# Kernel optimization log

Measured on AMD Instinct MI355X. Metric: run time of the kernel, lower is better.

The kernel has to match this reference:

```python
import jax, jax.numpy as jnp
import numpy as np

B, A, D, H = 16384, 16, 512, 512


def setup_inputs() -> dict:
    key = jax.random.key(0)
    ks = jax.random.split(key, 8)
    s = 1.0 / np.sqrt(D)
    sh = 1.0 / np.sqrt(H)
    return {
        "state": jax.random.normal(ks[0], (B, D), jnp.float32),
        "W1": jax.random.normal(ks[1], (A, D, H), jnp.float32) * s,
        "b1": jax.random.normal(ks[2], (A, H), jnp.float32) * s,
        "W2": jax.random.normal(ks[3], (A, H, H), jnp.float32) * sh,
        "b2": jax.random.normal(ks[4], (A, H), jnp.float32) * sh,
        "W3": jax.random.normal(ks[5], (A, H, 1), jnp.float32) * sh,
        "b3": jax.random.normal(ks[6], (A, 1), jnp.float32) * sh,
        "actions": jax.random.randint(ks[7], (B,), 0, A, jnp.int64),
    }


def reference(state, W1, b1, W2, b2, W3, b3, actions):
    # All per-action MLPs applied to every state as grouped/batched GEMMs.
    # h1, h2: [B, A, H]; out: [B, A, n_out]
    h1 = jax.nn.relu(jnp.einsum("bd,adh->bah", state, W1) + b1)
    h2 = jax.nn.relu(jnp.einsum("bah,ahk->bak", h1, W2) + b2)
    out = jnp.einsum("bah,ahk->bak", h2, W3) + b3  # [B, A, 1]
    # Gather the selected action's output per batch element -> [B, n_out]
    return jnp.take_along_axis(out, actions[:, None, None], axis=1)[:, 0, :]
```

## Files before the change

### kernel.cpp

```cpp
#include <hip/hip_runtime.h>
#include <hip/hip_bf16.h>
#include <stdint.h>

typedef __hip_bfloat16 bf16;
typedef float f32x4 __attribute__((ext_vector_type(4)));
typedef short bf16x8 __attribute__((ext_vector_type(8)));

#define NB 16384
#define NA 16
#define ND 512
#define NH 512
#define TR 80

#define W1S_OFF 0u
#define W2S_OFF 8388608u
#define PERM_OFF 16777216u
#define META_OFF 16842752u

__device__ __forceinline__ unsigned short f2b(float x) {
  unsigned int b = __float_as_uint(x);
  return (unsigned short)((b + 0x7FFFu + ((b >> 16) & 1u)) >> 16);
}

__global__ __launch_bounds__(256) void k_prep(const float* __restrict__ W1,
                                              const float* __restrict__ W2,
                                              bf16* __restrict__ W1s,
                                              bf16* __restrict__ W2s,
                                              const int* __restrict__ act,
                                              int* __restrict__ meta,
                                              int* __restrict__ perm) {
  __shared__ union {
    float tile[64][65];
    struct { int hist[16][256]; int off16[16]; } m;
  } lds;
  if (blockIdx.x == 2048) {
    int t = threadIdx.x;
    int lane = t & 63, wv = t >> 6;
#pragma unroll
    for (int i = 0; i < 16; ++i) lds.m.hist[i][t] = 0;
    __syncthreads();
    for (int j = 0; j < 64; ++j) {
      int a = act[t + (j << 8)] & 15;
      lds.m.hist[a][t]++;
    }
    __syncthreads();
    for (int q = 0; q < 4; ++q) {
      int a = (wv << 2) + q;
      int base = lane << 2;
      int v0 = lds.m.hist[a][base + 0];
      int v1 = lds.m.hist[a][base + 1];
      int v2 = lds.m.hist[a][base + 2];
      int v3 = lds.m.hist[a][base + 3];
      int s = v0 + v1 + v2 + v3;
      int incl = s;
#pragma unroll
      for (int d = 1; d < 64; d <<= 1) {
        int y = __shfl_up(incl, d);
        if (lane >= d) incl += y;
      }
      int excl = incl - s;
      lds.m.hist[a][base + 0] = excl;
      lds.m.hist[a][base + 1] = excl + v0;
      lds.m.hist[a][base + 2] = excl + v0 + v1;
      lds.m.hist[a][base + 3] = excl + v0 + v1 + v2;
      if (lane == 63) lds.m.off16[a] = incl;
    }
    __syncthreads();
    if (t == 0) {
      int o = 0;
      for (int aa = 0; aa < 16; ++aa) {
        int c = lds.m.off16[aa];
        meta[aa] = c;
        meta[16 + aa] = o;
        lds.m.off16[aa] = o;
        o += c;
      }
    }
    __syncthreads();
    for (int j = 0; j < 64; ++j) {
      int idx = t + (j << 8);
      int a = act[idx] & 15;
      int pos = lds.m.off16[a] + lds.m.hist[a][t]++;
      perm[pos] = idx;
    }
    return;
  }
  int j = blockIdx.x;
  int xcd = j & 7;
  int job = j >> 3;
  int mi = job >> 6;
  int m = (mi < 2) ? ((xcd << 1) + mi) : (NA + (xcd << 1) + (mi - 2));
  int tl = job & 63;
  int td = tl >> 3, th = tl & 7;
  const float* src = (m < NA) ? (W1 + (size_t)m * (ND * NH)) : (W2 + (size_t)(m - NA) * (ND * NH));
  char* dstb = (m < NA) ? ((char*)W1s + ((size_t)m << 19)) : ((char*)W2s + ((size_t)(m - NA) << 19));
  int t = threadIdx.x;
  int r = t >> 2, c0 = (t & 3) << 4;
  const float* sp = src + (size_t)(td * 64 + r) * NH + th * 64 + c0;
  float4 v0 = ((const float4*)sp)[0];
  float4 v1 = ((const float4*)sp)[1];
  float4 v2 = ((const float4*)sp)[2];
  float4 v3 = ((const float4*)sp)[3];
  float* tr = &lds.tile[r][c0];
  tr[0] = v0.x; tr[1] = v0.y; tr[2] = v0.z; tr[3] = v0.w;
  tr[4] = v1.x; tr[5] = v1.y; tr[6] = v1.z; tr[7] = v1.w;
  tr[8] = v2.x; tr[9] = v2.y; tr[10] = v2.z; tr[11] = v2.w;
  tr[12] = v3.x; tr[13] = v3.y; tr[14] = v3.z; tr[15] = v3.w;
  __syncthreads();
  int wv = t >> 6, l = t & 63;
  int l15b = l & 15, l4b = l >> 4;
#pragma unroll
  for (int kc = 0; kc < 2; ++kc) {
    union { unsigned short us[8]; uint4 q; } u;
#pragma unroll
    for (int i = 0; i < 8; ++i)
      u.us[i] = f2b(lds.tile[kc * 32 + l4b * 8 + i][wv * 16 + l15b]);
    int hb = th * 4 + wv;
    int kb = td * 2 + kc;
    *(uint4*)(dstb + ((size_t)(hb * 16 + kb) << 10) + (l << 4)) = u.q;
  }
}

__global__ __launch_bounds__(1024, 4) void k_main(
    const float* __restrict__ state, const float* __restrict__ b1,
    const float* __restrict__ b2, const float* __restrict__ W3,
    const float* __restrict__ b3, const bf16* __restrict__ W1s,
    const bf16* __restrict__ W2s, const int* __restrict__ perm,
    const int* __restrict__ meta, float* __restrict__ out) {
  extern __shared__ char smem[];
  char* Xs = smem;
  float* outbuf = (float*)(smem + 81920);

  int bid = blockIdx.x;
  int xcd = bid & 7, slot = bid >> 3;
  int a0 = xcd << 1;
  int n0 = meta[a0], n1 = meta[a0 + 1];
  int nt0 = (n0 + TR - 1) / TR, nt1 = (n1 + TR - 1) / TR;
  int a, t;
  if (slot < nt0) {
    a = a0; t = slot;
  } else if (slot < nt0 + nt1) {
    a = a0 + 1; t = slot - nt0;
  } else {
    return;
  }
  int rowbase = meta[16 + a] + t * TR;
  int nrows = meta[a] - t * TR;
  nrows = nrows > TR ? TR : nrows;

  int tid = threadIdx.x;
  int lane = tid & 63;
  int w = tid >> 6;
  int hw = w & 7;
  int ch = w >> 3;
  int bf0 = ch ? 3 : 0;
  int bfn = ch ? 2 : 3;
  int l15 = lane & 15, l4 = lane >> 4;

  const char* Wl = (const char*)W1s + ((size_t)a << 19) + (hw << 16) + (lane << 4);
  const char* Wl2 = (const char*)W2s + ((size_t)a << 19) + (hw << 16) + (lane << 4);

  bf16x8 A[2][4];
  bf16x8 Bc[3];
#pragma unroll
  for (int s = 0; s < 2; ++s)
#pragma unroll
    for (int hf = 0; hf < 4; ++hf)
      A[s][hf] = *(const bf16x8*)(Wl + (hf << 14) + (s << 10));

  {
#pragma unroll
    for (int it = 0; it < 10; ++it) {
      int c = tid + (it << 10);
      int row = c >> 7, chunk = c & 127;
      int gr = (row < nrows) ? perm[rowbase + row] : -1;
      float4 v = make_float4(0.f, 0.f, 0.f, 0.f);
      if (gr >= 0) v = *(const float4*)(state + (size_t)gr * ND + (chunk << 2));
      uint2 pk;
      pk.x = (unsigned)f2b(v.x) | ((unsigned)f2b(v.y) << 16);
      pk.y = (unsigned)f2b(v.z) | ((unsigned)f2b(v.w) << 16);
      *(uint2*)(Xs + row * 1024 + ((chunk << 3) ^ ((row & 7) << 4))) = pk;
    }
  }
  __syncthreads();

  uint2 h1p[12];

  {
    f32x4 acc[4][3] = {};
#pragma unroll
    for (int ks = 0; ks < 16; ++ks) {
#pragma unroll
      for (int bf = 0; bf < 3; ++bf) {
        if (bf < bfn) {
          int b = ((bf0 + bf) << 4) + l15;
          Bc[bf] = *(const bf16x8*)(Xs + b * 1024 + (((ks << 6) + (l4 << 4)) ^ ((b & 7) << 4)));
        }
      }
      __builtin_amdgcn_s_setprio(1);
#pragma unroll
      for (int hf = 0; hf < 4; ++hf)
#pragma unroll
        for (int bf = 0; bf < 3; ++bf)
          if (bf < bfn)
            acc[hf][bf] = __builtin_amdgcn_mfma_f32_16x16x32_bf16(A[ks & 1][hf], Bc[bf], acc[hf][bf], 0, 0, 0);
      __builtin_amdgcn_s_setprio(0);
      if (ks < 14) {
#pragma unroll
        for (int hf = 0; hf < 4; ++hf)
          A[ks & 1][hf] = *(const bf16x8*)(Wl + (hf << 14) + ((ks + 2) << 10));
      }
    }
#pragma unroll
    for (int s = 0; s < 2; ++s)
#pragma unroll
      for (int hf = 0; hf < 4; ++hf)
        A[s][hf] = *(const bf16x8*)(Wl2 + (hf << 14) + (s << 10));
#pragma unroll
    for (int hf = 0; hf < 4; ++hf) {
      int hb = (hw << 6) + (hf << 4) + (l4 << 2);
      float4 bias = *(const float4*)(b1 + (a << 9) + hb);
#pragma unroll
      for (int bf = 0; bf < 3; ++bf) {
        if (bf < bfn) {
          float x0 = fmaxf(acc[hf][bf][0] + bias.x, 0.f);
          float x1 = fmaxf(acc[hf][bf][1] + bias.y, 0.f);
          float x2 = fmaxf(acc[hf][bf][2] + bias.z, 0.f);
          float x3 = fmaxf(acc[hf][bf][3] + bias.w, 0.f);
          h1p[hf * 3 + bf].x = (unsigned)f2b(x0) | ((unsigned)f2b(x1) << 16);
          h1p[hf * 3 + bf].y = (unsigned)f2b(x2) | ((unsigned)f2b(x3) << 16);
        }
      }
    }
  }
  __syncthreads();
#pragma unroll
  for (int hf = 0; hf < 4; ++hf) {
    int hb2 = ((hw << 6) + (hf << 4) + (l4 << 2)) << 1;
#pragma unroll
    for (int bf = 0; bf < 3; ++bf) {
      if (bf < bfn) {
        int b = ((bf0 + bf) << 4) + l15;
        *(uint2*)(Xs + b * 1024 + (hb2 ^ ((b & 7) << 4))) = h1p[hf * 3 + bf];
      }
    }
  }
  __syncthreads();

  {
    f32x4 acc[4][3] = {};
#pragma unroll
    for (int ks = 0; ks < 16; ++ks) {
#pragma unroll
      for (int bf = 0; bf < 3; ++bf) {
        if (bf < bfn) {
          int b = ((bf0 + bf) << 4) + l15;
          Bc[bf] = *(const bf16x8*)(Xs + b * 1024 + (((ks << 6) + (l4 << 4)) ^ ((b & 7) << 4)));
        }
      }
      __builtin_amdgcn_s_setprio(1);
#pragma unroll
      for (int hf = 0; hf < 4; ++hf)
#pragma unroll
        for (int bf = 0; bf < 3; ++bf)
          if (bf < bfn)
            acc[hf][bf] = __builtin_amdgcn_mfma_f32_16x16x32_bf16(A[ks & 1][hf], Bc[bf], acc[hf][bf], 0, 0, 0);
      __builtin_amdgcn_s_setprio(0);
      if (ks < 14) {
#pragma unroll
        for (int hf = 0; hf < 4; ++hf)
          A[ks & 1][hf] = *(const bf16x8*)(Wl2 + (hf << 14) + ((ks + 2) << 10));
      }
    }
    float part[3] = {0.f, 0.f, 0.f};
#pragma unroll
    for (int hf = 0; hf < 4; ++hf) {
      int hb = (hw << 6) + (hf << 4) + (l4 << 2);
      float4 bias = *(const float4*)(b2 + (a << 9) + hb);
      float4 w3v = *(const float4*)(W3 + (a << 9) + hb);
#pragma unroll
      for (int bf = 0; bf < 3; ++bf) {
        if (bf < bfn) {
          part[bf] += fmaxf(acc[hf][bf][0] + bias.x, 0.f) * w3v.x +
                      fmaxf(acc[hf][bf][1] + bias.y, 0.f) * w3v.y +
                      fmaxf(acc[hf][bf][2] + bias.z, 0.f) * w3v.z +
                      fmaxf(acc[hf][bf][3] + bias.w, 0.f) * w3v.w;
        }
      }
    }
#pragma unroll
    for (int bf = 0; bf < 3; ++bf) {
      if (bf < bfn) {
        float p = part[bf];
        p += __shfl_xor(p, 16);
        p += __shfl_xor(p, 32);
        if (l4 == 0) outbuf[w * TR + ((bf0 + bf) << 4) + l15] = p;
      }
    }
  }
  __syncthreads();
  if (tid < nrows) {
    float s = b3[a];
    int wb = (tid < 48) ? 0 : 8;
#pragma unroll
    for (int ww = 0; ww < 8; ++ww) s += outbuf[(wb + ww) * TR + tid];
    out[perm[rowbase + tid]] = s;
  }
}

extern "C" void kernel_launch(void* const* d_in, const int* in_sizes, int n_in,
                              void* d_out, int out_size, void* d_ws, size_t ws_size,
                              hipStream_t stream) {
  const float* state = (const float*)d_in[0];
  const float* W1 = (const float*)d_in[1];
  const float* b1 = (const float*)d_in[2];
  const float* W2 = (const float*)d_in[3];
  const float* b2 = (const float*)d_in[4];
  const float* W3 = (const float*)d_in[5];
  const float* b3 = (const float*)d_in[6];
  const int* actions = (const int*)d_in[7];
  float* out = (float*)d_out;
  char* ws = (char*)d_ws;
  bf16* W1s = (bf16*)(ws + W1S_OFF);
  bf16* W2s = (bf16*)(ws + W2S_OFF);
  int* perm = (int*)(ws + PERM_OFF);
  int* meta = (int*)(ws + META_OFF);

  k_prep<<<2049, 256, 0, stream>>>(W1, W2, W1s, W2s, actions, meta, perm);
  hipFuncSetAttribute((const void*)k_main, hipFuncAttributeMaxDynamicSharedMemorySize, 87040);
  k_main<<<256, 1024, 87040, stream>>>(state, b1, b2, W3, b3, W1s, W2s, perm, meta, out);
}
```

Baseline: 59.57 us.

## Shrink row tile to 48 with 512-thread blocks and double grid

Reduces the per-block row tile from 80 to 48 rows and the block size from 1024 to 512 threads, so each of 8 waves owns a 64-column H slice and processes all three 16-row B fragments uniformly. The grid doubles to 512 blocks and LDS per block shrinks. The aim is to remove the uneven split across wave halves and get more blocks resident per CU. In exchange, each weight tile is reused across fewer rows, so weight traffic per row goes up. The grid of 512 blocks must cover ceil(n/48) tiles per action pair on each XCD slot.

```diff
diff --git a/kernel.cpp b/kernel.cpp
--- a/kernel.cpp
+++ b/kernel.cpp
@@ -10,7 +10,7 @@
 #define NA 16
 #define ND 512
 #define NH 512
-#define TR 80
+#define TR 48
 
 #define W1S_OFF 0u
 #define W2S_OFF 8388608u
@@ -121,7 +121,7 @@
   }
 }
 
-__global__ __launch_bounds__(1024, 4) void k_main(
+__global__ __launch_bounds__(512, 2) void k_main(
     const float* __restrict__ state, const float* __restrict__ b1,
     const float* __restrict__ b2, const float* __restrict__ W3,
     const float* __restrict__ b3, const bf16* __restrict__ W1s,
@@ -129,7 +129,7 @@
     const int* __restrict__ meta, float* __restrict__ out) {
   extern __shared__ char smem[];
   char* Xs = smem;
-  float* outbuf = (float*)(smem + 81920);
+  float* outbuf = (float*)(smem + 49152);
 
   int bid = blockIdx.x;
   int xcd = bid & 7, slot = bid >> 3;
@@ -151,14 +151,10 @@
   int tid = threadIdx.x;
   int lane = tid & 63;
   int w = tid >> 6;
-  int hw = w & 7;
-  int ch = w >> 3;
-  int bf0 = ch ? 3 : 0;
-  int bfn = ch ? 2 : 3;
   int l15 = lane & 15, l4 = lane >> 4;
 
-  const char* Wl = (const char*)W1s + ((size_t)a << 19) + (hw << 16) + (lane << 4);
-  const char* Wl2 = (const char*)W2s + ((size_t)a << 19) + (hw << 16) + (lane << 4);
+  const char* Wl = (const char*)W1s + ((size_t)a << 19) + (w << 16) + (lane << 4);
+  const char* Wl2 = (const char*)W2s + ((size_t)a << 19) + (w << 16) + (lane << 4);
 
   bf16x8 A[2][4];
   bf16x8 Bc[3];
@@ -170,8 +166,8 @@
 
   {
 #pragma unroll
-    for (int it = 0; it < 10; ++it) {
-      int c = tid + (it << 10);
+    for (int it = 0; it < 12; ++it) {
+      int c = tid + (it << 9);
       int row = c >> 7, chunk = c & 127;
       int gr = (row < nrows) ? perm[rowbase + row] : -1;
       float4 v = make_float4(0.f, 0.f, 0.f, 0.f);
@@ -192,18 +188,15 @@
     for (int ks = 0; ks < 16; ++ks) {
 #pragma unroll
       for (int bf = 0; bf < 3; ++bf) {
-        if (bf < bfn) {
-          int b = ((bf0 + bf) << 4) + l15;
-          Bc[bf] = *(const bf16x8*)(Xs + b * 1024 + (((ks << 6) + (l4 << 4)) ^ ((b & 7) << 4)));
-        }
+        int b = (bf << 4) + l15;
+        Bc[bf] = *(const bf16x8*)(Xs + b * 1024 + (((ks << 6) + (l4 << 4)) ^ ((b & 7) << 4)));
       }
       __builtin_amdgcn_s_setprio(1);
 #pragma unroll
       for (int hf = 0; hf < 4; ++hf)
 #pragma unroll
         for (int bf = 0; bf < 3; ++bf)
-          if (bf < bfn)
-            acc[hf][bf] = __builtin_amdgcn_mfma_f32_16x16x32_bf16(A[ks & 1][hf], Bc[bf], acc[hf][bf], 0, 0, 0);
+          acc[hf][bf] = __builtin_amdgcn_mfma_f32_16x16x32_bf16(A[ks & 1][hf], Bc[bf], acc[hf][bf], 0, 0, 0);
       __builtin_amdgcn_s_setprio(0);
       if (ks < 14) {
 #pragma unroll
@@ -218,31 +211,27 @@
         A[s][hf] = *(const bf16x8*)(Wl2 + (hf << 14) + (s << 10));
 #pragma unroll
     for (int hf = 0; hf < 4; ++hf) {
-      int hb = (hw << 6) + (hf << 4) + (l4 << 2);
+      int hb = (w << 6) + (hf << 4) + (l4 << 2);
       float4 bias = *(const float4*)(b1 + (a << 9) + hb);
 #pragma unroll
       for (int bf = 0; bf < 3; ++bf) {
-        if (bf < bfn) {
-          float x0 = fmaxf(acc[hf][bf][0] + bias.x, 0.f);
-          float x1 = fmaxf(acc[hf][bf][1] + bias.y, 0.f);
-          float x2 = fmaxf(acc[hf][bf][2] + bias.z, 0.f);
-          float x3 = fmaxf(acc[hf][bf][3] + bias.w, 0.f);
-          h1p[hf * 3 + bf].x = (unsigned)f2b(x0) | ((unsigned)f2b(x1) << 16);
-          h1p[hf * 3 + bf].y = (unsigned)f2b(x2) | ((unsigned)f2b(x3) << 16);
-        }
+        float x0 = fmaxf(acc[hf][bf][0] + bias.x, 0.f);
+        float x1 = fmaxf(acc[hf][bf][1] + bias.y, 0.f);
+        float x2 = fmaxf(acc[hf][bf][2] + bias.z, 0.f);
+        float x3 = fmaxf(acc[hf][bf][3] + bias.w, 0.f);
+        h1p[hf * 3 + bf].x = (unsigned)f2b(x0) | ((unsigned)f2b(x1) << 16);
+        h1p[hf * 3 + bf].y = (unsigned)f2b(x2) | ((unsigned)f2b(x3) << 16);
       }
     }
   }
   __syncthreads();
 #pragma unroll
   for (int hf = 0; hf < 4; ++hf) {
-    int hb2 = ((hw << 6) + (hf << 4) + (l4 << 2)) << 1;
+    int hb2 = ((w << 6) + (hf << 4) + (l4 << 2)) << 1;
 #pragma unroll
     for (int bf = 0; bf < 3; ++bf) {
-      if (bf < bfn) {
-        int b = ((bf0 + bf) << 4) + l15;
-        *(uint2*)(Xs + b * 1024 + (hb2 ^ ((b & 7) << 4))) = h1p[hf * 3 + bf];
-      }
+      int b = (bf << 4) + l15;
+      *(uint2*)(Xs + b * 1024 + (hb2 ^ ((b & 7) << 4))) = h1p[hf * 3 + bf];
     }
   }
   __syncthreads();
@@ -253,18 +242,15 @@
     for (int ks = 0; ks < 16; ++ks) {
 #pragma unroll
       for (int bf = 0; bf < 3; ++bf) {
-        if (bf < bfn) {
-          int b = ((bf0 + bf) << 4) + l15;
-          Bc[bf] = *(const bf16x8*)(Xs + b * 1024 + (((ks << 6) + (l4 << 4)) ^ ((b & 7) << 4)));
-        }
+        int b = (bf << 4) + l15;
+        Bc[bf] = *(const bf16x8*)(Xs + b * 1024 + (((ks << 6) + (l4 << 4)) ^ ((b & 7) << 4)));
       }
       __builtin_amdgcn_s_setprio(1);
 #pragma unroll
       for (int hf = 0; hf < 4; ++hf)
 #pragma unroll
         for (int bf = 0; bf < 3; ++bf)
-          if (bf < bfn)
-            acc[hf][bf] = __builtin_amdgcn_mfma_f32_16x16x32_bf16(A[ks & 1][hf], Bc[bf], acc[hf][bf], 0, 0, 0);
+          acc[hf][bf] = __builtin_amdgcn_mfma_f32_16x16x32_bf16(A[ks & 1][hf], Bc[bf], acc[hf][bf], 0, 0, 0);
       __builtin_amdgcn_s_setprio(0);
       if (ks < 14) {
 #pragma unroll
@@ -275,35 +261,30 @@
     float part[3] = {0.f, 0.f, 0.f};
 #pragma unroll
     for (int hf = 0; hf < 4; ++hf) {
-      int hb = (hw << 6) + (hf << 4) + (l4 << 2);
+      int hb = (w << 6) + (hf << 4) + (l4 << 2);
       float4 bias = *(const float4*)(b2 + (a << 9) + hb);
       float4 w3v = *(const float4*)(W3 + (a << 9) + hb);
 #pragma unroll
       for (int bf = 0; bf < 3; ++bf) {
-        if (bf < bfn) {
-          part[bf] += fmaxf(acc[hf][bf][0] + bias.x, 0.f) * w3v.x +
-                      fmaxf(acc[hf][bf][1] + bias.y, 0.f) * w3v.y +
-                      fmaxf(acc[hf][bf][2] + bias.z, 0.f) * w3v.z +
-                      fmaxf(acc[hf][bf][3] + bias.w, 0.f) * w3v.w;
-        }
+        part[bf] += fmaxf(acc[hf][bf][0] + bias.x, 0.f) * w3v.x +
+                    fmaxf(acc[hf][bf][1] + bias.y, 0.f) * w3v.y +
+                    fmaxf(acc[hf][bf][2] + bias.z, 0.f) * w3v.z +
+                    fmaxf(acc[hf][bf][3] + bias.w, 0.f) * w3v.w;
       }
     }
 #pragma unroll
     for (int bf = 0; bf < 3; ++bf) {
-      if (bf < bfn) {
-        float p = part[bf];
-        p += __shfl_xor(p, 16);
-        p += __shfl_xor(p, 32);
-        if (l4 == 0) outbuf[w * TR + ((bf0 + bf) << 4) + l15] = p;
-      }
+      float p = part[bf];
+      p += __shfl_xor(p, 16);
+      p += __shfl_xor(p, 32);
+      if (l4 == 0) outbuf[w * TR + (bf << 4) + l15] = p;
     }
   }
   __syncthreads();
   if (tid < nrows) {
     float s = b3[a];
-    int wb = (tid < 48) ? 0 : 8;
-#pragma unroll
-    for (int ww = 0; ww < 8; ++ww) s += outbuf[(wb + ww) * TR + tid];
+#pragma unroll
+    for (int ww = 0; ww < 8; ++ww) s += outbuf[ww * TR + tid];
     out[perm[rowbase + tid]] = s;
   }
 }
@@ -327,6 +308,6 @@
   int* meta = (int*)(ws + META_OFF);
 
   k_prep<<<2049, 256, 0, stream>>>(W1, W2, W1s, W2s, actions, meta, perm);
-  hipFuncSetAttribute((const void*)k_main, hipFuncAttributeMaxDynamicSharedMemorySize, 87040);
-  k_main<<<256, 1024, 87040, stream>>>(state, b1, b2, W3, b3, W1s, W2s, perm, meta, out);
+  hipFuncSetAttribute((const void*)k_main, hipFuncAttributeMaxDynamicSharedMemorySize, 50688);
+  k_main<<<512, 512, 50688, stream>>>(state, b1, b2, W3, b3, W1s, W2s, perm, meta, out);
 }
```

New measurement: 63.56 us. 1.07x slower.
